# Performance work log

Measured on AMD Instinct MI355X. Metric: run time of the kernel, lower is better.

The kernel has to match this reference:

```python
import jax, jax.numpy as jnp
import numpy as np

N = 1_000_000   # memory slots (current_size == memory_size)
D = 64          # embedding_dim == compressed_dim (required by the source code)
B = 64          # query batch
QBITS = 8       # quantization_bits


def setup_inputs() -> dict:
    key = jax.random.key(0)
    ks = jax.random.split(key, 6)
    return {
        "query": jax.random.normal(ks[0], (B, D), dtype=jnp.float32),
        "memory": jax.random.normal(ks[1], (N, D), dtype=jnp.float32),
        "attention_weights": jax.random.normal(ks[2], (N,), dtype=jnp.float32),
        "Wq": jax.random.normal(ks[3], (D, D), dtype=jnp.float32) / np.sqrt(D),
        "Wk": jax.random.normal(ks[4], (D, D), dtype=jnp.float32) / np.sqrt(D),
        "Wv": jax.random.normal(ks[5], (D, D), dtype=jnp.float32) / np.sqrt(D),
        "top_k": 5,
    }


def reference(query, memory, attention_weights, Wq, Wk, Wv, top_k):
    d = memory.shape[1]
    levels = jnp.float32(2 ** QBITS - 1)
    # _quantize_tensor / _dequantize_tensor round-trip on the stored memory
    mn = memory.min()
    mx = memory.max()
    scale = (mx - mn) / levels
    zero_point = -mn / scale
    mem_dq = (jnp.round(memory / scale + zero_point) - zero_point) * scale  # [N, D]

    q = query @ Wq.T                    # [B, D]
    keys = mem_dq @ Wk.T                # [N, D]
    values = mem_dq @ Wv.T              # [N, D]

    # attention scores + per-slot bias
    scores = q @ keys.T / np.float32(np.sqrt(d)) + attention_weights[None, :]  # [B, N]

    top_scores, top_idx = jax.lax.top_k(scores, top_k)   # [B, k]
    gathered = jnp.take(values, top_idx, axis=0)         # [B, k, D] irregular gather
    dist = jax.nn.softmax(top_scores, axis=-1)           # [B, k]
    out = jnp.einsum('bk,bkd->bd', dist, gathered)       # [B, D]
    return out
```

## Files before the change

### kernel.cpp

```cpp
#include <hip/hip_runtime.h>
#include <stdint.h>

constexpr int NROWS = 1000000;
constexpr int D = 64;
constexpr int B = 64;
constexpr int TOPK = 5;
constexpr int TBLK = 8;
constexpr int TRES = 16;
constexpr int NB2MAX = 1280;

typedef __attribute__((ext_vector_type(8))) short short8;
typedef __attribute__((ext_vector_type(4))) float floatx4;

#define OFF_QKF   512
#define OFF_QKB   16896
#define OFF_MM    25088
#define OFF_CAND  57856

__device__ __forceinline__ unsigned fkey(float x) {
    unsigned u = __float_as_uint(x);
    return (u & 0x80000000u) ? ~u : (u | 0x80000000u);
}
__device__ __forceinline__ float fkey_inv(unsigned k) {
    unsigned u = (k & 0x80000000u) ? (k ^ 0x80000000u) : ~k;
    return __uint_as_float(u);
}
__device__ __forceinline__ unsigned short f2bf_rne(float x) {
    unsigned u = __float_as_uint(x);
    u += 0x7fffu + ((u >> 16) & 1u);
    return (unsigned short)(u >> 16);
}

template<int K>
__device__ __forceinline__ void insert_key(unsigned long long (&ks)[K],
                                           unsigned long long key) {
    if (key > ks[K - 1]) {
        #pragma unroll
        for (int j = K - 1; j > 0; --j)
            ks[j] = (key > ks[j - 1]) ? ks[j - 1] : ((key > ks[j]) ? key : ks[j]);
        ks[0] = (key > ks[0]) ? key : ks[0];
    }
}

__global__ void k_qk(const float* __restrict__ query, const float* __restrict__ Wq,
                     const float* __restrict__ Wk,
                     float* __restrict__ qkf, unsigned short* __restrict__ qkb) {
    __shared__ float q[4][64];
    int t = threadIdx.x;
    int b0 = blockIdx.x * 4;
    int bq = t >> 6, d = t & 63;
    float s1 = 0.f;
    for (int e = 0; e < 64; e++) s1 += query[(b0 + bq) * 64 + e] * Wq[d * 64 + e];
    q[bq][d] = s1;
    __syncthreads();
    float v = 0.f;
    for (int dd = 0; dd < 64; dd++) v += q[bq][dd] * Wk[dd * 64 + d];
    v *= 0.125f;
    qkf[(b0 + bq) * 64 + d] = v;
    qkb[(b0 + bq) * 64 + d] = f2bf_rne(v);
}

__launch_bounds__(256, 5)
__global__ void k_score_mm(const float* __restrict__ mem, const float* __restrict__ aw,
                           const unsigned short* __restrict__ qkb,
                           unsigned long long* __restrict__ cand,
                           unsigned* __restrict__ part, int rowsPerBlock) {
    __shared__ __align__(16) char smem[26624];
    __shared__ float awt[64];
    __shared__ float swmn[4], swmx[4];
    unsigned short (*codes)[72] = (unsigned short (*)[72])smem;
    float (*scores)[68] = (float (*)[68])(smem + 9216);
    unsigned long long* cmerge = (unsigned long long*)smem;

    int t = threadIdx.x;
    int l15 = t & 15, quad = (t >> 4) & 3, w = t >> 6;
    int b = t & 63;

    short8 bq[4][2];
    #pragma unroll
    for (int bt = 0; bt < 4; bt++) {
        #pragma unroll
        for (int kb = 0; kb < 2; kb++)
            bq[bt][kb] = *(const short8*)(qkb + (bt * 16 + l15) * 64 + kb * 32 + quad * 8);
    }

    unsigned long long ks[TBLK];
    #pragma unroll
    for (int j = 0; j < TBLK; j++) ks[j] = 0ull;

    float mnv = 3.402823466e38f, mxv = -3.402823466e38f;

    int row0 = blockIdx.x * rowsPerBlock;
    int rowEnd = min(row0 + rowsPerBlock, NROWS);

    float4 pre[4];
    float preaw = 0.f;
    {
        int base = row0 < NROWS ? row0 : 0;
        #pragma unroll
        for (int i = 0; i < 4; i++) {
            int flat = (i * 256 + t) * 4;
            int g = base * 64 + flat;
            if (g > NROWS * 64 - 4) g = NROWS * 64 - 4;
            pre[i] = *(const float4*)(mem + g);
        }
        if (t < 64) {
            int ai = base + t; if (ai > NROWS - 1) ai = NROWS - 1;
            preaw = aw[ai];
        }
    }

    for (int base = row0; base < rowEnd; base += 64) {
        #pragma unroll
        for (int i = 0; i < 4; i++) {
            float4 v = pre[i];
            mnv = fminf(mnv, fminf(fminf(v.x, v.y), fminf(v.z, v.w)));
            mxv = fmaxf(mxv, fmaxf(fmaxf(v.x, v.y), fmaxf(v.z, v.w)));
            ushort4 c;
            c.x = f2bf_rne(v.x);
            c.y = f2bf_rne(v.y);
            c.z = f2bf_rne(v.z);
            c.w = f2bf_rne(v.w);
            int flat = (i * 256 + t) * 4;
            *(ushort4*)&codes[flat >> 6][flat & 63] = c;
        }
        if (t < 64) awt[t] = preaw;

        int nbase = (base + 64 < rowEnd) ? base + 64 : base;
        #pragma unroll
        for (int i = 0; i < 4; i++) {
            int flat = (i * 256 + t) * 4;
            int g = nbase * 64 + flat;
            if (g > NROWS * 64 - 4) g = NROWS * 64 - 4;
            pre[i] = *(const float4*)(mem + g);
        }
        if (t < 64) {
            int ai = nbase + t; if (ai > NROWS - 1) ai = NROWS - 1;
            preaw = aw[ai];
        }

        asm volatile("s_waitcnt lgkmcnt(0)" ::: "memory");
        __builtin_amdgcn_s_barrier();

        short8 a0 = *(const short8*)&codes[w * 16 + l15][quad * 8];
        short8 a1 = *(const short8*)&codes[w * 16 + l15][32 + quad * 8];
        float aw4[4];
        #pragma unroll
        for (int r = 0; r < 4; r++) aw4[r] = awt[w * 16 + quad * 4 + r];

        #pragma unroll
        for (int bt = 0; bt < 4; bt++) {
            floatx4 acc = {aw4[0], aw4[1], aw4[2], aw4[3]};
            acc = __builtin_amdgcn_mfma_f32_16x16x32_bf16(a0, bq[bt][0], acc, 0, 0, 0);
            acc = __builtin_amdgcn_mfma_f32_16x16x32_bf16(a1, bq[bt][1], acc, 0, 0, 0);
            *(floatx4*)&scores[bt * 16 + l15][w * 16 + quad * 4] = acc;
        }

        #pragma unroll
        for (int j = 0; j < 4; j++) {
            floatx4 v = *(const floatx4*)&scores[b][w * 16 + 4 * j];
            #pragma unroll
            for (int c2 = 0; c2 < 4; c2++) {
                int gr = base + w * 16 + 4 * j + c2;
                if (gr < rowEnd) {
                    unsigned long long key =
                        ((unsigned long long)fkey(v[c2]) << 32) | (unsigned)(~(unsigned)gr);
                    insert_key<TBLK>(ks, key);
                }
            }
        }

        asm volatile("s_waitcnt lgkmcnt(0)" ::: "memory");
        __builtin_amdgcn_s_barrier();
    }

    float mnw = mnv, mxw = mxv;
    #pragma unroll
    for (int o = 32; o > 0; o >>= 1) {
        mnw = fminf(mnw, __shfl_xor(mnw, o));
        mxw = fmaxf(mxw, __shfl_xor(mxw, o));
    }
    if ((t & 63) == 0) { swmn[w] = mnw; swmx[w] = mxw; }

    __syncthreads();
    #pragma unroll
    for (int j = 0; j < TBLK; j++) cmerge[t * TBLK + j] = ks[j];
    __syncthreads();
    if (t == 0) {
        float a = fminf(fminf(swmn[0], swmn[1]), fminf(swmn[2], swmn[3]));
        float b2 = fmaxf(fmaxf(swmx[0], swmx[1]), fmaxf(swmx[2], swmx[3]));
        part[blockIdx.x * 2 + 0] = fkey(a);
        part[blockIdx.x * 2 + 1] = fkey(b2);
    }
    if (t < 64) {
        unsigned long long ts[TBLK];
        #pragma unroll
        for (int j = 0; j < TBLK; j++) ts[j] = 0ull;
        for (int ww = 0; ww < 4; ww++)
            #pragma unroll
            for (int j = 0; j < TBLK; j++)
                insert_key<TBLK>(ts, cmerge[(ww * 64 + t) * TBLK + j]);
        #pragma unroll
        for (int j = 0; j < TBLK; j++)
            cand[((long long)blockIdx.x * 64 + t) * TBLK + j] = ts[j];
    }
}

__global__ void k_finalize(const unsigned long long* __restrict__ cand, int nb2,
                           const float* __restrict__ mem, const float* __restrict__ aw,
                           const float* __restrict__ Wv, const unsigned* __restrict__ part,
                           const float* __restrict__ qkf, float* __restrict__ out) {
    __shared__ unsigned long long lists[256][TRES];
    __shared__ float qkr[64];
    __shared__ int exid[TRES];
    __shared__ unsigned long long exkey[TRES];
    __shared__ float exsc[TRES];
    __shared__ float wsel[TOPK];
    __shared__ int isel[TOPK];
    __shared__ float su[64];
    __shared__ unsigned redmn[4], redmx[4];
    __shared__ float sscale[2];

    int t = threadIdx.x, b = blockIdx.x;
    int total = nb2 * TBLK;

    unsigned mnk = 0xFFFFFFFFu, mxk = 0u;
    for (int i = t; i < nb2; i += 256) {
        unsigned a = part[2 * i], c = part[2 * i + 1];
        mnk = a < mnk ? a : mnk;
        mxk = c > mxk ? c : mxk;
    }
    #pragma unroll
    for (int o = 32; o > 0; o >>= 1) {
        unsigned am = __shfl_xor(mnk, o); mnk = am < mnk ? am : mnk;
        unsigned ax = __shfl_xor(mxk, o); mxk = ax > mxk ? ax : mxk;
    }
    int w4 = t >> 6;
    if ((t & 63) == 0) { redmn[w4] = mnk; redmx[w4] = mxk; }

    unsigned long long loc[TRES];
    #pragma unroll
    for (int j = 0; j < TRES; j++) loc[j] = 0ull;
    for (int i = t; i < total; i += 256) {
        int blk = i / TBLK, j = i - blk * TBLK;
        insert_key<TRES>(loc, cand[((long long)blk * 64 + b) * TBLK + j]);
    }
    #pragma unroll
    for (int j = 0; j < TRES; j++) lists[t][j] = loc[j];
    if (t < 64) qkr[t] = qkf[b * 64 + t];
    __syncthreads();

    if (t == 255) {
        unsigned m0 = redmn[0], M0 = redmx[0];
        #pragma unroll
        for (int i = 1; i < 4; i++) {
            m0 = redmn[i] < m0 ? redmn[i] : m0;
            M0 = redmx[i] > M0 ? redmx[i] : M0;
        }
        float mnv = fkey_inv(m0), mxv = fkey_inv(M0);
        float scale = (mxv - mnv) / 255.0f;
        sscale[0] = scale;
        sscale[1] = -mnv / scale;
    }

    for (int s = 128; s > 0; s >>= 1) {
        if (t < s) {
            #pragma unroll
            for (int j = 0; j < TRES; j++) insert_key<TRES>(loc, lists[t + s][j]);
            #pragma unroll
            for (int j = 0; j < TRES; j++) lists[t][j] = loc[j];
        }
        __syncthreads();
    }
    if (t < TRES) {
        unsigned long long k = lists[0][t];
        exid[t] = k ? (int)(~(unsigned)k) : 0;
    }
    __syncthreads();

    float scale = sscale[0], zp = sscale[1];

    int lane = t & 63, w = t >> 6;
    for (int i = 0; i < 4; i++) {
        int c = w * 4 + i;
        int idx = exid[c];
        float m = mem[(long long)idx * 64 + lane];
        float dq = (rintf(m / scale + zp) - zp) * scale;
        float p2 = dq * qkr[lane];
        for (int o = 32; o > 0; o >>= 1) p2 += __shfl_xor(p2, o);
        if (lane == 0) {
            float ex = p2 + aw[idx];
            exsc[c] = ex;
            exkey[c] = ((unsigned long long)fkey(ex) << 32) | (unsigned)(~(unsigned)idx);
        }
    }
    __syncthreads();

    if (t == 0) {
        unsigned long long bnd = ~0ull;
        float ssel[TOPK];
        for (int p = 0; p < TOPK; p++) {
            unsigned long long best = 0ull; int bc = 0;
            for (int c = 0; c < TRES; c++) {
                unsigned long long k = exkey[c];
                if (k < bnd && k > best) { best = k; bc = c; }
            }
            bnd = best;
            ssel[p] = exsc[bc];
            isel[p] = exid[bc];
        }
        float Z = 0.f;
        for (int p = 0; p < TOPK; p++) { wsel[p] = expf(ssel[p] - ssel[0]); Z += wsel[p]; }
        for (int p = 0; p < TOPK; p++) wsel[p] /= Z;
    }
    __syncthreads();

    if (t < 64) {
        float u = 0.f;
        #pragma unroll
        for (int p = 0; p < TOPK; p++) {
            float m = mem[(long long)isel[p] * 64 + t];
            float dq = (rintf(m / scale + zp) - zp) * scale;
            u += wsel[p] * dq;
        }
        su[t] = u;
    }
    __syncthreads();
    if (t < 64) {
        float o = 0.f;
        #pragma unroll
        for (int e = 0; e < 64; e++) o += su[e] * Wv[t * 64 + e];
        out[b * 64 + t] = o;
    }
}

extern "C" void kernel_launch(void* const* d_in, const int* in_sizes, int n_in,
                              void* d_out, int out_size, void* d_ws, size_t ws_size,
                              hipStream_t stream) {
    const float* query = (const float*)d_in[0];
    const float* mem   = (const float*)d_in[1];
    const float* aw    = (const float*)d_in[2];
    const float* Wq    = (const float*)d_in[3];
    const float* Wk    = (const float*)d_in[4];
    const float* Wv    = (const float*)d_in[5];
    float* out = (float*)d_out;

    char* ws = (char*)d_ws;
    float* qkf     = (float*)(ws + OFF_QKF);
    unsigned short* qkb = (unsigned short*)(ws + OFF_QKB);
    unsigned* part = (unsigned*)(ws + OFF_MM);
    unsigned long long* cand = (unsigned long long*)(ws + OFF_CAND);

    int nb2 = NB2MAX;
    size_t need = (size_t)OFF_CAND + (size_t)nb2 * 64 * TBLK * 8;
    if (ws_size < need) {
        size_t avail = ws_size > OFF_CAND ? ws_size - OFF_CAND : 0;
        nb2 = (int)(avail / ((size_t)64 * TBLK * 8));
        if (nb2 < 8) nb2 = 8;
        if (nb2 > NB2MAX) nb2 = NB2MAX;
    }
    int rpb = (NROWS + nb2 - 1) / nb2;

    k_qk<<<16, 256, 0, stream>>>(query, Wq, Wk, qkf, qkb);
    k_score_mm<<<nb2, 256, 0, stream>>>(mem, aw, qkb, cand, part, rpb);
    k_finalize<<<B, 256, 0, stream>>>(cand, nb2, mem, aw, Wv, part, qkf, out);
}
```

Measured before the change: 477.9 us.

## Make score kernel wave-independent with register MFMA operands and top-2 selection

The score kernel now gives each wave its own contiguous row range. Memory rows are loaded straight into the bf16 MFMA A-fragment registers, which removes the LDS staging of codes and scores and the per-tile block barriers. Each lane keeps only a top-2 per batch column; these lists are merged across quads with shuffles and then across waves into a top-4 per block, with TBLK reduced and the block count and occupancy hint adjusted. This cuts selection and synchronisation work per row, but it keeps fewer candidates per row group, so the top-k recall relies on the exact rescoring in finalize.

Measured after the change: 415.1 us. 13.1% less time.

```diff
diff --git a/kernel.cpp b/kernel.cpp
--- a/kernel.cpp
+++ b/kernel.cpp
@@ -5,12 +5,13 @@
 constexpr int D = 64;
 constexpr int B = 64;
 constexpr int TOPK = 5;
-constexpr int TBLK = 8;
+constexpr int TBLK = 4;
 constexpr int TRES = 16;
-constexpr int NB2MAX = 1280;
+constexpr int NB2MAX = 1024;
 
 typedef __attribute__((ext_vector_type(8))) short short8;
 typedef __attribute__((ext_vector_type(4))) float floatx4;
+typedef unsigned long long u64;
 
 #define OFF_QKF   512
 #define OFF_QKB   16896
@@ -32,14 +33,20 @@
 }
 
 template<int K>
-__device__ __forceinline__ void insert_key(unsigned long long (&ks)[K],
-                                           unsigned long long key) {
+__device__ __forceinline__ void insert_key(u64 (&ks)[K], u64 key) {
     if (key > ks[K - 1]) {
         #pragma unroll
         for (int j = K - 1; j > 0; --j)
             ks[j] = (key > ks[j - 1]) ? ks[j - 1] : ((key > ks[j]) ? key : ks[j]);
         ks[0] = (key > ks[0]) ? key : ks[0];
     }
+}
+
+__device__ __forceinline__ void insert2(u64& a, u64& b, u64 key) {
+    u64 hi = key > a ? key : a;
+    u64 lo = key > a ? a : key;
+    b = lo > b ? lo : b;
+    a = hi;
 }
 
 __global__ void k_qk(const float* __restrict__ query, const float* __restrict__ Wq,
@@ -60,21 +67,16 @@
     qkb[(b0 + bq) * 64 + d] = f2bf_rne(v);
 }
 
-__launch_bounds__(256, 5)
+__launch_bounds__(256, 4)
 __global__ void k_score_mm(const float* __restrict__ mem, const float* __restrict__ aw,
                            const unsigned short* __restrict__ qkb,
-                           unsigned long long* __restrict__ cand,
-                           unsigned* __restrict__ part, int rowsPerBlock) {
-    __shared__ __align__(16) char smem[26624];
-    __shared__ float awt[64];
+                           u64* __restrict__ cand,
+                           unsigned* __restrict__ part, int wrows) {
+    __shared__ u64 mrg[4][4][16][2];
     __shared__ float swmn[4], swmx[4];
-    unsigned short (*codes)[72] = (unsigned short (*)[72])smem;
-    float (*scores)[68] = (float (*)[68])(smem + 9216);
-    unsigned long long* cmerge = (unsigned long long*)smem;
 
     int t = threadIdx.x;
     int l15 = t & 15, quad = (t >> 4) & 3, w = t >> 6;
-    int b = t & 63;
 
     short8 bq[4][2];
     #pragma unroll
@@ -84,108 +86,102 @@
             bq[bt][kb] = *(const short8*)(qkb + (bt * 16 + l15) * 64 + kb * 32 + quad * 8);
     }
 
-    unsigned long long ks[TBLK];
-    #pragma unroll
-    for (int j = 0; j < TBLK; j++) ks[j] = 0ull;
+    u64 Ltop[4], Lsec[4];
+    #pragma unroll
+    for (int bt = 0; bt < 4; bt++) { Ltop[bt] = 0ull; Lsec[bt] = 0ull; }
 
     float mnv = 3.402823466e38f, mxv = -3.402823466e38f;
 
-    int row0 = blockIdx.x * rowsPerBlock;
-    int rowEnd = min(row0 + rowsPerBlock, NROWS);
-
-    float4 pre[4];
-    float preaw = 0.f;
-    {
-        int base = row0 < NROWS ? row0 : 0;
-        #pragma unroll
-        for (int i = 0; i < 4; i++) {
-            int flat = (i * 256 + t) * 4;
-            int g = base * 64 + flat;
-            if (g > NROWS * 64 - 4) g = NROWS * 64 - 4;
-            pre[i] = *(const float4*)(mem + g);
-        }
-        if (t < 64) {
-            int ai = base + t; if (ai > NROWS - 1) ai = NROWS - 1;
-            preaw = aw[ai];
-        }
-    }
-
-    for (int base = row0; base < rowEnd; base += 64) {
-        #pragma unroll
-        for (int i = 0; i < 4; i++) {
-            float4 v = pre[i];
-            mnv = fminf(mnv, fminf(fminf(v.x, v.y), fminf(v.z, v.w)));
-            mxv = fmaxf(mxv, fmaxf(fmaxf(v.x, v.y), fmaxf(v.z, v.w)));
-            ushort4 c;
-            c.x = f2bf_rne(v.x);
-            c.y = f2bf_rne(v.y);
-            c.z = f2bf_rne(v.z);
-            c.w = f2bf_rne(v.w);
-            int flat = (i * 256 + t) * 4;
-            *(ushort4*)&codes[flat >> 6][flat & 63] = c;
-        }
-        if (t < 64) awt[t] = preaw;
-
-        int nbase = (base + 64 < rowEnd) ? base + 64 : base;
-        #pragma unroll
-        for (int i = 0; i < 4; i++) {
-            int flat = (i * 256 + t) * 4;
-            int g = nbase * 64 + flat;
-            if (g > NROWS * 64 - 4) g = NROWS * 64 - 4;
-            pre[i] = *(const float4*)(mem + g);
-        }
-        if (t < 64) {
-            int ai = nbase + t; if (ai > NROWS - 1) ai = NROWS - 1;
-            preaw = aw[ai];
-        }
-
-        asm volatile("s_waitcnt lgkmcnt(0)" ::: "memory");
-        __builtin_amdgcn_s_barrier();
-
-        short8 a0 = *(const short8*)&codes[w * 16 + l15][quad * 8];
-        short8 a1 = *(const short8*)&codes[w * 16 + l15][32 + quad * 8];
-        float aw4[4];
-        #pragma unroll
-        for (int r = 0; r < 4; r++) aw4[r] = awt[w * 16 + quad * 4 + r];
+    int gw = blockIdx.x * 4 + w;
+    int wbeg = gw * wrows;
+    int wend = min(wbeg + wrows, NROWS);
+    int span = wend - wbeg;
+    int nt = span > 0 ? (span >> 4) : 0;
+
+    const char* pbase = (const char*)mem + (size_t)wbeg * 256 + (size_t)(l15 * 256 + quad * 32);
+    const float* abase = aw + wbeg + quad * 4;
+
+    float4 p0, p1, p2, p3, pa;
+    if (nt > 0) {
+        p0 = *(const float4*)(pbase);
+        p1 = *(const float4*)(pbase + 16);
+        p2 = *(const float4*)(pbase + 128);
+        p3 = *(const float4*)(pbase + 144);
+        pa = *(const float4*)(abase);
+    }
+
+    for (int it = 0; it < nt; ++it) {
+        float4 c0 = p0, c1 = p1, c2 = p2, c3 = p3;
+        float aw0 = pa.x, aw1 = pa.y, aw2 = pa.z, aw3 = pa.w;
+
+        int nx = (it + 1 < nt) ? (it + 1) : (nt - 1);
+        const char* pn = pbase + (size_t)nx * 4096;
+        p0 = *(const float4*)(pn);
+        p1 = *(const float4*)(pn + 16);
+        p2 = *(const float4*)(pn + 128);
+        p3 = *(const float4*)(pn + 144);
+        pa = *(const float4*)(abase + nx * 16);
+
+        mnv = fminf(mnv, fminf(fminf(c0.x, c0.y), fminf(c0.z, c0.w)));
+        mxv = fmaxf(mxv, fmaxf(fmaxf(c0.x, c0.y), fmaxf(c0.z, c0.w)));
+        mnv = fminf(mnv, fminf(fminf(c1.x, c1.y), fminf(c1.z, c1.w)));
+        mxv = fmaxf(mxv, fmaxf(fmaxf(c1.x, c1.y), fmaxf(c1.z, c1.w)));
+        mnv = fminf(mnv, fminf(fminf(c2.x, c2.y), fminf(c2.z, c2.w)));
+        mxv = fmaxf(mxv, fmaxf(fmaxf(c2.x, c2.y), fmaxf(c2.z, c2.w)));
+        mnv = fminf(mnv, fminf(fminf(c3.x, c3.y), fminf(c3.z, c3.w)));
+        mxv = fmaxf(mxv, fmaxf(fmaxf(c3.x, c3.y), fmaxf(c3.z, c3.w)));
+
+        short8 a0, a1;
+        a0[0] = (short)f2bf_rne(c0.x); a0[1] = (short)f2bf_rne(c0.y);
+        a0[2] = (short)f2bf_rne(c0.z); a0[3] = (short)f2bf_rne(c0.w);
+        a0[4] = (short)f2bf_rne(c1.x); a0[5] = (short)f2bf_rne(c1.y);
+        a0[6] = (short)f2bf_rne(c1.z); a0[7] = (short)f2bf_rne(c1.w);
+        a1[0] = (short)f2bf_rne(c2.x); a1[1] = (short)f2bf_rne(c2.y);
+        a1[2] = (short)f2bf_rne(c2.z); a1[3] = (short)f2bf_rne(c2.w);
+        a1[4] = (short)f2bf_rne(c3.x); a1[5] = (short)f2bf_rne(c3.y);
+        a1[6] = (short)f2bf_rne(c3.z); a1[7] = (short)f2bf_rne(c3.w);
+
+        int gr = wbeg + it * 16 + quad * 4;
 
         #pragma unroll
         for (int bt = 0; bt < 4; bt++) {
-            floatx4 acc = {aw4[0], aw4[1], aw4[2], aw4[3]};
+            floatx4 acc = {aw0, aw1, aw2, aw3};
             acc = __builtin_amdgcn_mfma_f32_16x16x32_bf16(a0, bq[bt][0], acc, 0, 0, 0);
             acc = __builtin_amdgcn_mfma_f32_16x16x32_bf16(a1, bq[bt][1], acc, 0, 0, 0);
-            *(floatx4*)&scores[bt * 16 + l15][w * 16 + quad * 4] = acc;
-        }
-
-        #pragma unroll
-        for (int j = 0; j < 4; j++) {
-            floatx4 v = *(const floatx4*)&scores[b][w * 16 + 4 * j];
             #pragma unroll
-            for (int c2 = 0; c2 < 4; c2++) {
-                int gr = base + w * 16 + 4 * j + c2;
-                if (gr < rowEnd) {
-                    unsigned long long key =
-                        ((unsigned long long)fkey(v[c2]) << 32) | (unsigned)(~(unsigned)gr);
-                    insert_key<TBLK>(ks, key);
-                }
+            for (int r = 0; r < 4; r++) {
+                u64 key = ((u64)fkey(acc[r]) << 32) | (unsigned)(~(unsigned)(gr + r));
+                insert2(Ltop[bt], Lsec[bt], key);
             }
         }
-
-        asm volatile("s_waitcnt lgkmcnt(0)" ::: "memory");
-        __builtin_amdgcn_s_barrier();
-    }
-
-    float mnw = mnv, mxw = mxv;
+    }
+
     #pragma unroll
     for (int o = 32; o > 0; o >>= 1) {
-        mnw = fminf(mnw, __shfl_xor(mnw, o));
-        mxw = fmaxf(mxw, __shfl_xor(mxw, o));
-    }
-    if ((t & 63) == 0) { swmn[w] = mnw; swmx[w] = mxw; }
-
-    __syncthreads();
-    #pragma unroll
-    for (int j = 0; j < TBLK; j++) cmerge[t * TBLK + j] = ks[j];
-    __syncthreads();
+        mnv = fminf(mnv, __shfl_xor(mnv, o));
+        mxv = fmaxf(mxv, __shfl_xor(mxv, o));
+    }
+    if ((t & 63) == 0) { swmn[w] = mnv; swmx[w] = mxv; }
+
+    #pragma unroll
+    for (int bt = 0; bt < 4; bt++) {
+        #pragma unroll
+        for (int dlt = 16; dlt <= 32; dlt <<= 1) {
+            u64 ka = __shfl_xor(Ltop[bt], dlt);
+            u64 kb = __shfl_xor(Lsec[bt], dlt);
+            insert2(Ltop[bt], Lsec[bt], ka);
+            insert2(Ltop[bt], Lsec[bt], kb);
+        }
+    }
+    if ((t & 48) == 0) {
+        #pragma unroll
+        for (int bt = 0; bt < 4; bt++) {
+            mrg[w][bt][l15][0] = Ltop[bt];
+            mrg[w][bt][l15][1] = Lsec[bt];
+        }
+    }
+    __syncthreads();
+
     if (t == 0) {
         float a = fminf(fminf(swmn[0], swmn[1]), fminf(swmn[2], swmn[3]));
         float b2 = fmaxf(fmaxf(swmx[0], swmx[1]), fmaxf(swmx[2], swmx[3]));
@@ -193,27 +189,29 @@
         part[blockIdx.x * 2 + 1] = fkey(b2);
     }
     if (t < 64) {
-        unsigned long long ts[TBLK];
+        u64 ts[TBLK];
         #pragma unroll
         for (int j = 0; j < TBLK; j++) ts[j] = 0ull;
-        for (int ww = 0; ww < 4; ww++)
-            #pragma unroll
-            for (int j = 0; j < TBLK; j++)
-                insert_key<TBLK>(ts, cmerge[(ww * 64 + t) * TBLK + j]);
+        int bt = t >> 4, l = t & 15;
+        #pragma unroll
+        for (int w2 = 0; w2 < 4; w2++) {
+            insert_key<TBLK>(ts, mrg[w2][bt][l][0]);
+            insert_key<TBLK>(ts, mrg[w2][bt][l][1]);
+        }
         #pragma unroll
         for (int j = 0; j < TBLK; j++)
             cand[((long long)blockIdx.x * 64 + t) * TBLK + j] = ts[j];
     }
 }
 
-__global__ void k_finalize(const unsigned long long* __restrict__ cand, int nb2,
+__global__ void k_finalize(const u64* __restrict__ cand, int nb2,
                            const float* __restrict__ mem, const float* __restrict__ aw,
                            const float* __restrict__ Wv, const unsigned* __restrict__ part,
                            const float* __restrict__ qkf, float* __restrict__ out) {
-    __shared__ unsigned long long lists[256][TRES];
+    __shared__ u64 lists[256][TRES];
     __shared__ float qkr[64];
     __shared__ int exid[TRES];
-    __shared__ unsigned long long exkey[TRES];
+    __shared__ u64 exkey[TRES];
     __shared__ float exsc[TRES];
     __shared__ float wsel[TOPK];
     __shared__ int isel[TOPK];
@@ -238,7 +236,7 @@
     int w4 = t >> 6;
     if ((t & 63) == 0) { redmn[w4] = mnk; redmx[w4] = mxk; }
 
-    unsigned long long loc[TRES];
+    u64 loc[TRES];
     #pragma unroll
     for (int j = 0; j < TRES; j++) loc[j] = 0ull;
     for (int i = t; i < total; i += 256) {
@@ -273,7 +271,7 @@
         __syncthreads();
     }
     if (t < TRES) {
-        unsigned long long k = lists[0][t];
+        u64 k = lists[0][t];
         exid[t] = k ? (int)(~(unsigned)k) : 0;
     }
     __syncthreads();
@@ -291,18 +289,18 @@
         if (lane == 0) {
             float ex = p2 + aw[idx];
             exsc[c] = ex;
-            exkey[c] = ((unsigned long long)fkey(ex) << 32) | (unsigned)(~(unsigned)idx);
+            exkey[c] = ((u64)fkey(ex) << 32) | (unsigned)(~(unsigned)idx);
         }
     }
     __syncthreads();
 
     if (t == 0) {
-        unsigned long long bnd = ~0ull;
+        u64 bnd = ~0ull;
         float ssel[TOPK];
         for (int p = 0; p < TOPK; p++) {
-            unsigned long long best = 0ull; int bc = 0;
+            u64 best = 0ull; int bc = 0;
             for (int c = 0; c < TRES; c++) {
-                unsigned long long k = exkey[c];
+                u64 k = exkey[c];
                 if (k < bnd && k > best) { best = k; bc = c; }
             }
             bnd = best;
@@ -349,7 +347,7 @@
     float* qkf     = (float*)(ws + OFF_QKF);
     unsigned short* qkb = (unsigned short*)(ws + OFF_QKB);
     unsigned* part = (unsigned*)(ws + OFF_MM);
-    unsigned long long* cand = (unsigned long long*)(ws + OFF_CAND);
+    u64* cand = (u64*)(ws + OFF_CAND);
 
     int nb2 = NB2MAX;
     size_t need = (size_t)OFF_CAND + (size_t)nb2 * 64 * TBLK * 8;
@@ -359,9 +357,10 @@
         if (nb2 < 8) nb2 = 8;
         if (nb2 > NB2MAX) nb2 = NB2MAX;
     }
-    int rpb = (NROWS + nb2 - 1) / nb2;
+    int waves = nb2 * 4;
+    int wrows = ((NROWS + waves - 1) / waves + 15) / 16 * 16;
 
     k_qk<<<16, 256, 0, stream>>>(query, Wq, Wk, qkf, qkb);
-    k_score_mm<<<nb2, 256, 0, stream>>>(mem, aw, qkb, cand, part, rpb);
+    k_score_mm<<<nb2, 256, 0, stream>>>(mem, aw, qkb, cand, part, wrows);
     k_finalize<<<B, 256, 0, stream>>>(cand, nb2, mem, aw, Wv, part, qkf, out);
 }
```
